# Performance work log

Hardware: AMD Instinct MI355X
Metric: run time of the kernel (lower is better)

## Reference

```python
import jax, jax.numpy as jnp
import numpy as np

N, E, R, H = 20000, 320000, 8, 4
KG, CC = 128, 4
IN, HID, OUT = 256, 256, 256  # in_channels = KG + 128 (GCN out)
HO1, HO2 = HID // H, OUT // H  # per-head out channels
SLOPE_ACT = 0.01   # nn.LeakyReLU default
SLOPE_ATT = 0.2    # RGATConv negative_slope default


def gcn_conv(x, W, b, src, dst):
    """PyG GCNConv: add self loops, symmetric norm, x@W, scatter-sum, +bias."""
    n = x.shape[0]
    loop = jnp.arange(n, dtype=src.dtype)
    s = jnp.concatenate([src, loop])
    d = jnp.concatenate([dst, loop])
    deg = jnp.zeros((n,), x.dtype).at[d].add(1.0)
    dis = jnp.where(deg > 0, jax.lax.rsqrt(jnp.maximum(deg, 1.0)), 0.0)
    norm = dis[s] * dis[d]                        # [E+N]
    h = x @ W                                     # [n, out]
    out = jax.ops.segment_sum(norm[:, None] * h[s], d, num_segments=n)
    return out + b


def rgat_conv(x, W, q, k, b, src, dst, edge_type, heads, oc):
    """PyG RGATConv (additive-self-attention, across-relation, dim=1, concat)."""
    n = x.shape[0]
    xw = jnp.einsum('ni,rio->rno', x, W)          # [R, n, heads*oc]
    out_i = xw[edge_type, dst]                    # [E, heads*oc]
    out_j = xw[edge_type, src]                    # [E, heads*oc]
    qi = out_i @ q                                # [E, heads]
    kj = out_j @ k                                # [E, heads]
    alpha = jax.nn.leaky_relu(qi + kj, SLOPE_ATT)
    # softmax over incoming edges per destination node (across-relation)
    amax = jax.ops.segment_max(alpha, dst, num_segments=n)[dst]
    ex = jnp.exp(alpha - amax)
    denom = jax.ops.segment_sum(ex, dst, num_segments=n)[dst]
    alpha = ex / denom                            # [E, heads]
    e = src.shape[0]
    msg = (alpha[:, :, None] * out_j.reshape(e, heads, oc)).reshape(e, heads * oc)
    out = jax.ops.segment_sum(msg, dst, num_segments=n) + b
    return out, alpha


def setup_inputs() -> dict:
    key = jax.random.key(0)
    ks = jax.random.split(key, 16)
    d = {}
    d['kg_emb'] = jax.random.normal(ks[0], (N, KG), jnp.float32)
    d['ccle0'] = jax.random.normal(ks[1], (N, CC), jnp.float32)
    d['gcn_w1'] = jax.random.normal(ks[2], (CC, 32), jnp.float32) / np.float32(np.sqrt(CC))
    d['gcn_b1'] = jnp.zeros((32,), jnp.float32)
    d['gcn_w2'] = jax.random.normal(ks[3], (32, 128), jnp.float32) / np.float32(np.sqrt(32))
    d['gcn_b2'] = jnp.zeros((128,), jnp.float32)
    d['rgat1_w'] = jax.random.normal(ks[4], (R, IN, HID), jnp.float32) / np.float32(np.sqrt(IN))
    d['rgat1_q'] = jax.random.normal(ks[5], (HID, H), jnp.float32) / np.float32(np.sqrt(HID))
    d['rgat1_k'] = jax.random.normal(ks[6], (HID, H), jnp.float32) / np.float32(np.sqrt(HID))
    d['rgat1_b'] = jnp.zeros((HID,), jnp.float32)
    d['rgat2_w'] = jax.random.normal(ks[7], (R, HID, OUT), jnp.float32) / np.float32(np.sqrt(HID))
    d['rgat2_q'] = jax.random.normal(ks[8], (OUT, H), jnp.float32) / np.float32(np.sqrt(OUT))
    d['rgat2_k'] = jax.random.normal(ks[9], (OUT, H), jnp.float32) / np.float32(np.sqrt(OUT))
    d['rgat2_b'] = jnp.zeros((OUT,), jnp.float32)
    d['lin_w'] = jax.random.normal(ks[10], (IN, OUT), jnp.float32) / np.float32(np.sqrt(IN))
    d['lin_b'] = jnp.zeros((OUT,), jnp.float32)
    d['edge_index'] = jax.random.randint(ks[11], (2, E), 0, N, jnp.int32)
    d['edge_type'] = jax.random.randint(ks[12], (E,), 0, R, jnp.int32)
    return d


def reference(kg_emb, ccle0, gcn_w1, gcn_b1, gcn_w2, gcn_b2,
              rgat1_w, rgat1_q, rgat1_k, rgat1_b,
              rgat2_w, rgat2_q, rgat2_k, rgat2_b,
              lin_w, lin_b, edge_index, edge_type):
    src, dst = edge_index[0], edge_index[1]
    # ccle_layer: GCN(4->32) -> LeakyReLU -> GCN(32->128)
    c = gcn_conv(ccle0, gcn_w1, gcn_b1, src, dst)
    c = jax.nn.leaky_relu(c, SLOPE_ACT)
    c = gcn_conv(c, gcn_w2, gcn_b2, src, dst)
    # node_id = arange(N): concat(kg_emb, ccle_out)
    x0 = jnp.concatenate([kg_emb, c], axis=1)     # [N, IN]
    h, a1 = rgat_conv(x0, rgat1_w, rgat1_q, rgat1_k, rgat1_b,
                      src, dst, edge_type, H, HO1)
    h = jax.nn.leaky_relu(h, SLOPE_ACT)           # dropout p=0 -> identity
    h, a2 = rgat_conv(h, rgat2_w, rgat2_q, rgat2_k, rgat2_b,
                      src, dst, edge_type, H, HO2)
    out = h + (x0 @ lin_w + lin_b)                # residual through self.lin
    return out, a1, a2
```

## Files before the change

### kernel.cpp

```cpp
#include <hip/hip_runtime.h>
#include <cstdint>

static constexpr int N = 20000;
static constexpr int E = 320000;
static constexpr int R = 8;
static constexpr int H = 4;
static constexpr int C = 256;

using short8 = __attribute__((ext_vector_type(8))) short;
using f32x4  = __attribute__((ext_vector_type(4))) float;
using us4    = __attribute__((ext_vector_type(4))) unsigned short;

__device__ __forceinline__ float lrelu(float x, float s) { return x >= 0.f ? x : s * x; }
__device__ __forceinline__ unsigned short f2bf(float f) {
    unsigned u = __float_as_uint(f);
    unsigned r = (u + 0x7FFFu + ((u >> 16) & 1u)) >> 16;
    return (unsigned short)r;
}
__device__ __forceinline__ float bf2f(unsigned short s) {
    return __uint_as_float(((unsigned)s) << 16);
}

__device__ __forceinline__ void gl2l16(const unsigned short* g, unsigned short* l) {
    __builtin_amdgcn_global_load_lds(
        (const __attribute__((address_space(1))) unsigned int*)g,
        (__attribute__((address_space(3))) unsigned int*)l, 16, 0, 0);
}

__global__ void k_zero_int(int* p, int n) {
    int i = blockIdx.x * blockDim.x + threadIdx.x;
    if (i < n) p[i] = 0;
}

__global__ void k_count(const int* __restrict__ ei, int* __restrict__ cnt) {
    int e = blockIdx.x * blockDim.x + threadIdx.x;
    if (e < E) atomicAdd(&cnt[ei[E + e]], 1);
}

__global__ __launch_bounds__(256) void k_scan_a(const int* __restrict__ cnt,
                                                int* __restrict__ loc,
                                                int* __restrict__ bsum) {
    __shared__ int sm[256];
    int t = threadIdx.x;
    int idx = blockIdx.x * 256 + t;
    int v = (idx < N) ? cnt[idx] : 0;
    sm[t] = v;
    __syncthreads();
#pragma unroll
    for (int off = 1; off < 256; off <<= 1) {
        int u = (t >= off) ? sm[t - off] : 0;
        __syncthreads();
        if (t >= off) sm[t] += u;
        __syncthreads();
    }
    if (idx < N) loc[idx] = sm[t] - v;
    if (t == 255) bsum[blockIdx.x] = sm[255];
}

__global__ __launch_bounds__(256) void k_scan_c(const int* __restrict__ cnt,
                                                const int* __restrict__ loc,
                                                const int* __restrict__ bsum,
                                                int* __restrict__ rowptr,
                                                int* __restrict__ cursor,
                                                float* __restrict__ dis) {
    __shared__ int wsum[4];
    __shared__ int smoff;
    int t = threadIdx.x;
    int part = 0;
    for (int j = t; j < blockIdx.x; j += 256) part += bsum[j];
#pragma unroll
    for (int d = 1; d < 64; d <<= 1) part += __shfl_xor(part, d);
    if ((t & 63) == 0) wsum[t >> 6] = part;
    __syncthreads();
    if (t == 0) smoff = wsum[0] + wsum[1] + wsum[2] + wsum[3];
    __syncthreads();
    int base = smoff;
    int idx = blockIdx.x * 256 + t;
    if (idx == 0) rowptr[N] = E;
    if (idx >= N) return;
    int run = base + loc[idx];
    rowptr[idx] = run;
    cursor[idx] = run;
    dis[idx] = rsqrtf((float)cnt[idx] + 1.0f);
}

__global__ void k_scatter(const int* __restrict__ ei, const int* __restrict__ et,
                          int* __restrict__ cursor, int* __restrict__ csr_se,
                          int* __restrict__ csr_eid) {
    int e = blockIdx.x * blockDim.x + threadIdx.x;
    if (e >= E) return;
    int d = ei[E + e];
    int pos = atomicAdd(&cursor[d], 1);
    csr_se[pos] = (et[e] << 16) | ei[e];
    csr_eid[pos] = e;
}

__global__ void k_h1(const float* __restrict__ x, const float* __restrict__ W,
                     float* __restrict__ h) {
    int idx = blockIdx.x * blockDim.x + threadIdx.x;
    if (idx >= N * 32) return;
    int n = idx >> 5, f = idx & 31;
    const float* xr = x + n * 4;
    float acc = 0.f;
#pragma unroll
    for (int c = 0; c < 4; ++c) acc += xr[c] * W[c * 32 + f];
    h[idx] = acc;
}

__global__ void k_agg32(const int* __restrict__ rowptr, const int* __restrict__ csr_se,
                        const float* __restrict__ dis, const float* __restrict__ h,
                        const float* __restrict__ b, float* __restrict__ c) {
    int idx = blockIdx.x * blockDim.x + threadIdx.x;
    if (idx >= N * 32) return;
    int d = idx >> 5, f = idx & 31;
    int beg = rowptr[d], end = rowptr[d + 1];
    float acc = 0.f;
    for (int i = beg; i < end; ++i) {
        int s = csr_se[i] & 0xFFFF;
        acc += dis[s] * h[s * 32 + f];
    }
    float dd = dis[d];
    c[idx] = dd * acc + dd * dd * h[idx] + b[f];
}

__global__ void k_h2kg(const float* __restrict__ c1, const float* __restrict__ W,
                       const float* __restrict__ kg, unsigned short* __restrict__ h,
                       float* __restrict__ x0, unsigned short* __restrict__ xb0) {
    int idx = blockIdx.x * blockDim.x + threadIdx.x;
    if (idx >= N * 128) return;
    int n = idx >> 7, f = idx & 127;
    const float* cr = c1 + n * 32;
    float acc = 0.f;
    for (int c = 0; c < 32; ++c) acc += lrelu(cr[c], 0.01f) * W[c * 128 + f];
    h[idx] = f2bf(acc);
    float v = kg[idx];
    x0[n * 256 + f] = v;
    xb0[n * 256 + f] = f2bf(v);
}

__global__ void k_agg128(const int* __restrict__ rowptr, const int* __restrict__ csr_se,
                         const float* __restrict__ dis,
                         const unsigned short* __restrict__ h,
                         const float* __restrict__ b, float* __restrict__ x0,
                         unsigned short* __restrict__ xb0) {
    int idx = blockIdx.x * blockDim.x + threadIdx.x;
    if (idx >= N * 128) return;
    int d = idx >> 7, f = idx & 127;
    int beg = rowptr[d], end = rowptr[d + 1];
    float acc = 0.f;
    int i = beg;
    for (; i + 2 <= end; i += 2) {
        int s0 = csr_se[i] & 0xFFFF;
        int s1 = csr_se[i + 1] & 0xFFFF;
        float d0 = dis[s0], d1 = dis[s1];
        float v0 = bf2f(h[s0 * 128 + f]), v1 = bf2f(h[s1 * 128 + f]);
        acc += d0 * v0 + d1 * v1;
    }
    if (i < end) {
        int s = csr_se[i] & 0xFFFF;
        acc += dis[s] * bf2f(h[s * 128 + f]);
    }
    float dd = dis[d];
    float v = dd * acc + dd * dd * bf2f(h[d * 128 + f]) + b[f];
    x0[d * 256 + 128 + f] = v;
    xb0[d * 256 + 128 + f] = f2bf(v);
}

__global__ __launch_bounds__(256) void k_wqkb(const float* __restrict__ W,
                                              const float* __restrict__ q,
                                              const float* __restrict__ kmat,
                                              unsigned short* __restrict__ wqkb) {
    int w = (blockIdx.x * blockDim.x + threadIdx.x) >> 6;
    int lane = threadIdx.x & 63;
    int r = w >> 8, i = w & 255;
    const float* wr = W + ((size_t)(r * 256 + i)) * 256;
    float4 a = *(const float4*)(wr + lane * 4);
    float aq0 = 0.f, aq1 = 0.f, aq2 = 0.f, aq3 = 0.f;
    float ak0 = 0.f, ak1 = 0.f, ak2 = 0.f, ak3 = 0.f;
    int o = lane * 4;
    const float av[4] = {a.x, a.y, a.z, a.w};
#pragma unroll
    for (int j = 0; j < 4; ++j) {
        float4 qv = *(const float4*)(q + (o + j) * 4);
        float4 kv = *(const float4*)(kmat + (o + j) * 4);
        aq0 += av[j] * qv.x; aq1 += av[j] * qv.y;
        aq2 += av[j] * qv.z; aq3 += av[j] * qv.w;
        ak0 += av[j] * kv.x; ak1 += av[j] * kv.y;
        ak2 += av[j] * kv.z; ak3 += av[j] * kv.w;
    }
#pragma unroll
    for (int d = 1; d < 64; d <<= 1) {
        aq0 += __shfl_xor(aq0, d); aq1 += __shfl_xor(aq1, d);
        aq2 += __shfl_xor(aq2, d); aq3 += __shfl_xor(aq3, d);
        ak0 += __shfl_xor(ak0, d); ak1 += __shfl_xor(ak1, d);
        ak2 += __shfl_xor(ak2, d); ak3 += __shfl_xor(ak3, d);
    }
    if (lane == 0) {
        int nq = r * 4, nk = 32 + r * 4;
        wqkb[(nq + 0) * 256 + i] = f2bf(aq0);
        wqkb[(nq + 1) * 256 + i] = f2bf(aq1);
        wqkb[(nq + 2) * 256 + i] = f2bf(aq2);
        wqkb[(nq + 3) * 256 + i] = f2bf(aq3);
        wqkb[(nk + 0) * 256 + i] = f2bf(ak0);
        wqkb[(nk + 1) * 256 + i] = f2bf(ak1);
        wqkb[(nk + 2) * 256 + i] = f2bf(ak2);
        wqkb[(nk + 3) * 256 + i] = f2bf(ak3);
    }
}

#define QP 264
__global__ __launch_bounds__(256) void k_qnkn_mfma(
    const unsigned short* __restrict__ xb, const unsigned short* __restrict__ wqkb,
    float* __restrict__ qn, float* __restrict__ kn)
{
    __shared__ unsigned short Ws[64 * QP];
    int t = threadIdx.x;
    {
        int r = t >> 2, off = (t & 3) * 64;
#pragma unroll
        for (int i = 0; i < 8; ++i)
            *(uint4*)(&Ws[r * QP + off + i * 8]) =
                *(const uint4*)(wqkb + r * 256 + off + i * 8);
    }
    __syncthreads();
    int wave = t >> 6, lane = t & 63;
    int lrow = lane & 15, kq = lane >> 4;
    int mw = blockIdx.x * 64 + wave * 16;
    int gm = mw + lrow;
    int gmc = gm < N ? gm : N - 1;

    f32x4 acc[4];
#pragma unroll
    for (int j = 0; j < 4; ++j) acc[j] = (f32x4){0.f, 0.f, 0.f, 0.f};

    for (int k0 = 0; k0 < 8; ++k0) {
        short8 af = *(const short8*)(xb + (size_t)gmc * 256 + k0 * 32 + kq * 8);
#pragma unroll
        for (int j = 0; j < 4; ++j) {
            short8 bf4 = *(const short8*)(&Ws[(j * 16 + lrow) * QP + k0 * 32 + kq * 8]);
            acc[j] = __builtin_amdgcn_mfma_f32_16x16x32_bf16(bf4, af, acc[j], 0, 0, 0);
        }
    }
    if (gm < N) {
#pragma unroll
        for (int j = 0; j < 4; ++j) {
            int colb = j * 16 + kq * 4;
            float4 v = {acc[j][0], acc[j][1], acc[j][2], acc[j][3]};
            if (colb < 32) *(float4*)(qn + (size_t)gm * 32 + colb) = v;
            else           *(float4*)(kn + (size_t)gm * 32 + (colb - 32)) = v;
        }
    }
}

__global__ void k_soft(const int* __restrict__ rowptr, const int* __restrict__ csr_se,
                       const int* __restrict__ csr_eid,
                       const float* __restrict__ qn, const float* __restrict__ kn,
                       float* __restrict__ alpha_csr, float* __restrict__ aout) {
    int wid = (blockIdx.x * blockDim.x + threadIdx.x) >> 6;
    int lane = threadIdx.x & 63;
    if (wid >= N) return;
    int d = wid;
    int beg = rowptr[d], end = rowptr[d + 1];
    if (beg >= end) return;
    int slot = lane >> 2, h = lane & 3;
    int nc = (end - beg + 15) >> 4;
    const float* qrow = qn + d * 32;

    auto rawv = [&](int i) {
        int se = csr_se[i];
        int tt = se >> 16, s = se & 0xFFFF;
        return lrelu(qrow[tt * 4 + h] + kn[s * 32 + tt * 4 + h], 0.2f);
    };

    float av[4];
    float m = -1e30f;
    for (int c = 0; c < nc; ++c) {
        int i = beg + c * 16 + slot;
        float v = (i < end) ? rawv(i) : -1e30f;
        if (c < 4) av[c] = v;
        m = fmaxf(m, v);
    }
    m = fmaxf(m, __shfl_xor(m, 4));
    m = fmaxf(m, __shfl_xor(m, 8));
    m = fmaxf(m, __shfl_xor(m, 16));
    m = fmaxf(m, __shfl_xor(m, 32));

    float sum = 0.f;
    for (int c = 0; c < nc; ++c) {
        int i = beg + c * 16 + slot;
        float ex = 0.f;
        if (i < end) {
            float v = (c < 4) ? av[c] : rawv(i);
            ex = expf(v - m);
        }
        if (c < 4) av[c] = ex;
        sum += ex;
    }
    sum += __shfl_xor(sum, 4);
    sum += __shfl_xor(sum, 8);
    sum += __shfl_xor(sum, 16);
    sum += __shfl_xor(sum, 32);
    float inv = 1.f / sum;

    for (int c = 0; c < nc; ++c) {
        int i = beg + c * 16 + slot;
        if (i < end) {
            float ex = (c < 4) ? av[c] : expf(rawv(i) - m);
            float a = ex * inv;
            alpha_csr[i * 4 + h] = a;
            aout[csr_eid[i] * 4 + h] = a;
        }
    }
}

__global__ __launch_bounds__(256) void k_soft_gather(
    const int* __restrict__ rowptr, const int* __restrict__ csr_se,
    const int* __restrict__ csr_eid,
    const float* __restrict__ qn, const float* __restrict__ kn,
    const unsigned short* __restrict__ xw,
    const float* __restrict__ bias, float* __restrict__ out,
    unsigned short* __restrict__ xbout, float* __restrict__ aout,
    int first, int act)
{
    int node = blockIdx.x * 4 + (threadIdx.x >> 6);
    if (node >= N) return;
    int lane = threadIdx.x & 63;
    int slot = lane >> 2, h = lane & 3;
    int hsel = lane >> 4;
    int beg = rowptr[node], end = rowptr[node + 1];
    float ax = 0.f, ay = 0.f, az = 0.f, aw = 0.f;
    const unsigned short* xwl = xw + lane * 4;

    if (beg < end) {
        int nc = (end - beg + 15) >> 4;
        const float* qrow = qn + node * 32;
        auto rawv = [&](int i) {
            int se = csr_se[i];
            int tt = se >> 16, s = se & 0xFFFF;
            return lrelu(qrow[tt * 4 + h] + kn[s * 32 + tt * 4 + h], 0.2f);
        };

        float av[4];
        float m = -1e30f;
        for (int c = 0; c < nc; ++c) {
            int i = beg + c * 16 + slot;
            float v = (i < end) ? rawv(i) : -1e30f;
            if (c < 4) av[c] = v;
            m = fmaxf(m, v);
        }
        m = fmaxf(m, __shfl_xor(m, 4));
        m = fmaxf(m, __shfl_xor(m, 8));
        m = fmaxf(m, __shfl_xor(m, 16));
        m = fmaxf(m, __shfl_xor(m, 32));

        float sum = 0.f;
        for (int c = 0; c < nc; ++c) {
            int i = beg + c * 16 + slot;
            float ex = 0.f;
            if (i < end) {
                float v = (c < 4) ? av[c] : rawv(i);
                ex = expf(v - m);
            }
            if (c < 4) av[c] = ex;
            sum += ex;
        }
        sum += __shfl_xor(sum, 4);
        sum += __shfl_xor(sum, 8);
        sum += __shfl_xor(sum, 16);
        sum += __shfl_xor(sum, 32);
        float inv = 1.f / sum;

        for (int c = 0; c < nc; ++c) {
            int i = beg + c * 16 + slot;
            float a = 0.f;
            int se = 0;
            if (i < end) {
                float ex = (c < 4) ? av[c] : expf(rawv(i) - m);
                a = ex * inv;
                se = csr_se[i];
                aout[csr_eid[i] * 4 + h] = a;
            }
            int ne = end - (beg + c * 16);
            if (ne > 16) ne = 16;
            for (int e = 0; e < ne; ++e) {
                float ag = __shfl(a, (e << 2) | hsel);
                int seg  = __shfl(se, e << 2);
                int tt = seg >> 16, s = seg & 0xFFFF;
                uint2 pv = *(const uint2*)(xwl + ((size_t)tt * N + s) * 256);
                ax += ag * __uint_as_float(pv.x << 16);
                ay += ag * __uint_as_float(pv.x & 0xFFFF0000u);
                az += ag * __uint_as_float(pv.y << 16);
                aw += ag * __uint_as_float(pv.y & 0xFFFF0000u);
            }
        }
    }

    float* o = out + (size_t)node * 256 + lane * 4;
    float vx, vy, vz, vw;
    if (first) {
        float4 b = *(const float4*)(bias + lane * 4);
        vx = ax + b.x; vy = ay + b.y; vz = az + b.z; vw = aw + b.w;
    } else {
        float4 q = *(const float4*)o;
        vx = q.x + ax; vy = q.y + ay; vz = q.z + az; vw = q.w + aw;
    }
    if (act) {
        vx = lrelu(vx, 0.01f); vy = lrelu(vy, 0.01f);
        vz = lrelu(vz, 0.01f); vw = lrelu(vw, 0.01f);
        us4 xv = {f2bf(vx), f2bf(vy), f2bf(vz), f2bf(vw)};
        *(us4*)(xbout + (size_t)node * 256 + lane * 4) = xv;
    }
    float4 v = {vx, vy, vz, vw};
    *(float4*)o = v;
}

#define WTP 72
__global__ __launch_bounds__(256) void k_wconv_t(const float* __restrict__ W,
                                                 unsigned short* __restrict__ Wt) {
    int bid = blockIdx.x;
    int z = bid >> 4;
    int tile = bid & 15;
    int k0 = (tile >> 2) * 64, n0 = (tile & 3) * 64;
    __shared__ unsigned short T[64 * WTP];
    int t = threadIdx.x;
    const float* Wz = W + ((size_t)z << 16);
    int r = t >> 4;
    int cs = (t & 15) * 4;
#pragma unroll
    for (int rr = 0; rr < 4; ++rr) {
        int k = r + rr * 16;
        float4 v = *(const float4*)(Wz + (size_t)(k0 + k) * 256 + n0 + cs);
        T[(cs + 0) * WTP + k] = f2bf(v.x);
        T[(cs + 1) * WTP + k] = f2bf(v.y);
        T[(cs + 2) * WTP + k] = f2bf(v.z);
        T[(cs + 3) * WTP + k] = f2bf(v.w);
    }
    __syncthreads();
    int n = t >> 2, ck = (t & 3) * 16;
    unsigned short* dst = Wt + ((size_t)z << 16) + (size_t)(n0 + n) * 256 + k0 + ck;
    const unsigned short* srcp = T + n * WTP + ck;
    *(uint4*)(dst) = *(const uint4*)(srcp);
    *(uint4*)(dst + 8) = *(const uint4*)(srcp + 8);
}

#define TM 128
#define TN 128
__global__ __launch_bounds__(256) void gemm_mfma4(
    const unsigned short* __restrict__ A, const unsigned short* __restrict__ Bt,
    unsigned short* __restrict__ Cbf, float* __restrict__ Cf,
    const float* __restrict__ bias, const float* __restrict__ bias2,
    int M, int NZ, int NT, int MT, int zlin)
{
    __shared__ unsigned short As[128 * 32];
    __shared__ unsigned short Bs[128 * 32];

    int bi = blockIdx.x;
    int cx = bi & 7;
    int g = bi >> 3;
    int per = NZ * NT;
    int mh = g / per;
    int j  = g % per;
    int mt = mh * 8 + cx;
    if (mt >= MT) return;
    int z  = j % NZ;
    int nb = j / NZ;
    int m0 = mt * TM;
    int n0 = nb * TN;

    const unsigned short* Bz = Bt + ((size_t)z << 16);
    int t = threadIdx.x;
    int wave = t >> 6, lane = t & 63;
    int wr = wave >> 1, wc = wave & 1;
    int lrow = lane & 15, kq = lane >> 4;

    int sr0 = (wave * 2 + 0) * 16 + (lane >> 2);
    int sr1 = (wave * 2 + 1) * 16 + (lane >> 2);
    int sc = (((lane & 3) ^ ((lane >> 3) & 3))) * 8;
    int gm0 = m0 + sr0; if (gm0 >= M) gm0 = M - 1;
    int gm1 = m0 + sr1; if (gm1 >= M) gm1 = M - 1;
    const unsigned short* gA0 = A + (size_t)gm0 * 256 + sc;
    const unsigned short* gA1 = A + (size_t)gm1 * 256 + sc;
    const unsigned short* gB0 = Bz + (size_t)(n0 + sr0) * 256 + sc;
    const unsigned short* gB1 = Bz + (size_t)(n0 + sr1) * 256 + sc;
    unsigned short* lA0 = &As[(wave * 2 + 0) * 512];
    unsigned short* lA1 = &As[(wave * 2 + 1) * 512];
    unsigned short* lB0 = &Bs[(wave * 2 + 0) * 512];
    unsigned short* lB1 = &Bs[(wave * 2 + 1) * 512];

    int rg = (kq ^ ((lrow >> 1) & 3)) * 8;

    f32x4 acc[4][4];
#pragma unroll
    for (int i = 0; i < 4; ++i)
#pragma unroll
        for (int jj = 0; jj < 4; ++jj) acc[i][jj] = (f32x4){0.f, 0.f, 0.f, 0.f};

    for (int k0 = 0; k0 < 256; k0 += 32) {
        gl2l16(gA0 + k0, lA0);
        gl2l16(gA1 + k0, lA1);
        gl2l16(gB0 + k0, lB0);
        gl2l16(gB1 + k0, lB1);
        __syncthreads();
        short8 af[4], bf4[4];
#pragma unroll
        for (int i = 0; i < 4; ++i)
            af[i] = *(const short8*)(&As[(wr * 64 + i * 16 + lrow) * 32 + rg]);
#pragma unroll
        for (int jj = 0; jj < 4; ++jj)
            bf4[jj] = *(const short8*)(&Bs[(wc * 64 + jj * 16 + lrow) * 32 + rg]);
#pragma unroll
        for (int i = 0; i < 4; ++i)
#pragma unroll
            for (int jj = 0; jj < 4; ++jj)
                acc[i][jj] = __builtin_amdgcn_mfma_f32_16x16x32_bf16(bf4[jj], af[i],
                                                                     acc[i][jj], 0, 0, 0);
        __syncthreads();
    }
    if (z == zlin) {
#pragma unroll
        for (int i = 0; i < 4; ++i) {
            int gm = m0 + wr * 64 + i * 16 + lrow;
            if (gm >= M) continue;
#pragma unroll
            for (int jj = 0; jj < 4; ++jj) {
                int gnb = n0 + wc * 64 + jj * 16 + kq * 4;
                float4 b1 = *(const float4*)(bias + gnb);
                float4 b2 = *(const float4*)(bias2 + gnb);
                float4 v = {acc[i][jj][0] + b1.x + b2.x,
                            acc[i][jj][1] + b1.y + b2.y,
                            acc[i][jj][2] + b1.z + b2.z,
                            acc[i][jj][3] + b1.w + b2.w};
                *(float4*)(Cf + (size_t)gm * 256 + gnb) = v;
            }
        }
    } else {
#pragma unroll
        for (int i = 0; i < 4; ++i) {
            int gm = m0 + wr * 64 + i * 16 + lrow;
            if (gm >= M) continue;
#pragma unroll
            for (int jj = 0; jj < 4; ++jj) {
                int gnb = n0 + wc * 64 + jj * 16 + kq * 4;
                us4 v = {f2bf(acc[i][jj][0]), f2bf(acc[i][jj][1]),
                         f2bf(acc[i][jj][2]), f2bf(acc[i][jj][3])};
                *(us4*)(Cbf + ((size_t)z * M + gm) * 256 + gnb) = v;
            }
        }
    }
}

__global__ __launch_bounds__(256) void k_msg_gather(
    const int* __restrict__ rowptr, const int* __restrict__ csr_se,
    const float* __restrict__ alpha_csr, const unsigned short* __restrict__ xw,
    const float* __restrict__ bias, float* __restrict__ out,
    unsigned short* __restrict__ xbout, int r0, int r1, int first, int act) {
    int node = blockIdx.x * 4 + (threadIdx.x >> 6);
    if (node >= N) return;
    int lane = threadIdx.x & 63;
    int hsel = lane >> 4;
    int beg = rowptr[node], end = rowptr[node + 1];
    float ax = 0.f, ay = 0.f, az = 0.f, aw = 0.f;
    const unsigned short* xwl = xw + lane * 4;

    for (int i = beg; i < end; ++i) {
        int se = csr_se[i];
        int tt = se >> 16;
        if (tt >= r0 && tt < r1) {
            int s = se & 0xFFFF;
            float a = alpha_csr[i * 4 + hsel];
            uint2 pv = *(const uint2*)(xwl + ((size_t)(tt - r0) * N + s) * 256);
            ax += a * __uint_as_float(pv.x << 16);
            ay += a * __uint_as_float(pv.x & 0xFFFF0000u);
            az += a * __uint_as_float(pv.y << 16);
            aw += a * __uint_as_float(pv.y & 0xFFFF0000u);
        }
    }

    float* o = out + (size_t)node * 256 + lane * 4;
    float vx, vy, vz, vw;
    if (first) {
        float4 b = *(const float4*)(bias + lane * 4);
        vx = ax + b.x; vy = ay + b.y; vz = az + b.z; vw = aw + b.w;
    } else {
        float4 q = *(const float4*)o;
        vx = q.x + ax; vy = q.y + ay; vz = q.z + az; vw = q.w + aw;
    }
    if (act) {
        vx = lrelu(vx, 0.01f); vy = lrelu(vy, 0.01f);
        vz = lrelu(vz, 0.01f); vw = lrelu(vw, 0.01f);
        us4 xv = {f2bf(vx), f2bf(vy), f2bf(vz), f2bf(vw)};
        *(us4*)(xbout + (size_t)node * 256 + lane * 4) = xv;
    }
    float4 v = {vx, vy, vz, vw};
    *(float4*)o = v;
}

extern "C" void kernel_launch(void* const* d_in, const int* in_sizes, int n_in,
                              void* d_out, int out_size, void* d_ws, size_t ws_size,
                              hipStream_t stream) {
    const float* kg   = (const float*)d_in[0];
    const float* cc0  = (const float*)d_in[1];
    const float* gw1  = (const float*)d_in[2];
    const float* gb1  = (const float*)d_in[3];
    const float* gw2  = (const float*)d_in[4];
    const float* gb2  = (const float*)d_in[5];
    const float* r1w  = (const float*)d_in[6];
    const float* r1q  = (const float*)d_in[7];
    const float* r1k  = (const float*)d_in[8];
    const float* r1b  = (const float*)d_in[9];
    const float* r2w  = (const float*)d_in[10];
    const float* r2q  = (const float*)d_in[11];
    const float* r2k  = (const float*)d_in[12];
    const float* r2b  = (const float*)d_in[13];
    const float* linw = (const float*)d_in[14];
    const float* linb = (const float*)d_in[15];
    const int*   ei   = (const int*)d_in[16];
    const int*   et   = (const int*)d_in[17];

    float* out = (float*)d_out;
    float* a1  = out + (size_t)N * C;
    float* a2  = a1 + (size_t)E * H;

    float* ws = (float*)d_ws;
    size_t off = 0;
    float* dis  = ws + off; off += N;
    float* h1   = ws + off; off += (size_t)N * 32;
    float* c1   = ws + off; off += (size_t)N * 32;
    unsigned short* h2b = (unsigned short*)(ws + off); off += (size_t)N * 64;
    float* x0   = ws + off; off += (size_t)N * C;
    float* hmid = ws + off; off += (size_t)N * C;
    float* qn   = ws + off; off += (size_t)N * R * H;
    float* kn   = ws + off; off += (size_t)N * R * H;
    int* cnt     = (int*)(ws + off); off += N;
    int* rowptr  = (int*)(ws + off); off += N + 1;
    int* cursor  = (int*)(ws + off); off += N;
    int* scanloc = (int*)(ws + off); off += N;
    int* scanbs  = (int*)(ws + off); off += 256;
    int* csr_se  = (int*)(ws + off); off += E;
    int* csr_eid = (int*)(ws + off); off += E;
    float* alpha = ws + off; off += (size_t)E * H;
    unsigned short* xb0 = (unsigned short*)(ws + off); off += (size_t)N * 128;
    unsigned short* xb1 = (unsigned short*)(ws + off); off += (size_t)N * 128;
    unsigned short* wt  = (unsigned short*)(ws + off); off += (size_t)(R + 1) * 32768;
    unsigned short* wtl = wt + ((size_t)R << 16);
    unsigned short* wqkb = (unsigned short*)(ws + off); off += 8192;
    unsigned short* xwb = (unsigned short*)(ws + off);

    size_t fixedB = off * 4;
    int K = R;
    if (ws_size > fixedB) {
        size_t kmax = (ws_size - fixedB) / ((size_t)N * C * 2);
        if (kmax < (size_t)K) K = (int)kmax;
    } else {
        K = 1;
    }
    if (K < 1) K = 1;

    const int B = 256;
    auto cdiv = [](long a, long b) { return (int)((a + b - 1) / b); };
    const int MT = cdiv(N, TM);
    const int NT = C / TN;
    const int NB = cdiv(N, 256);

    k_zero_int<<<cdiv(N, B), B, 0, stream>>>(cnt, N);
    k_count<<<cdiv(E, B), B, 0, stream>>>(ei, cnt);
    k_scan_a<<<NB, 256, 0, stream>>>(cnt, scanloc, scanbs);
    k_scan_c<<<NB, 256, 0, stream>>>(cnt, scanloc, scanbs, rowptr, cursor, dis);
    k_scatter<<<cdiv(E, B), B, 0, stream>>>(ei, et, cursor, csr_se, csr_eid);

    k_h1<<<cdiv((long)N * 32, B), B, 0, stream>>>(cc0, gw1, h1);
    k_agg32<<<cdiv((long)N * 32, B), B, 0, stream>>>(rowptr, csr_se, dis, h1, gb1, c1);
    k_h2kg<<<cdiv((long)N * 128, B), B, 0, stream>>>(c1, gw2, kg, h2b, x0, xb0);
    k_agg128<<<cdiv((long)N * 128, B), B, 0, stream>>>(rowptr, csr_se, dis, h2b,
                                                       gb2, x0, xb0);

    auto rgat = [&](unsigned short* xb, const float* W,
                    const float* q, const float* kk, const float* b,
                    float* obuf, unsigned short* xbout, float* aout,
                    int first, int act, int lin, float* linout,
                    const float* lb1, const float* lb2) {
        k_wqkb<<<512, 256, 0, stream>>>(W, q, kk, wqkb);
        k_qnkn_mfma<<<cdiv(N, 64), B, 0, stream>>>(xb, wqkb, qn, kn);
        k_wconv_t<<<R * 16, 256, 0, stream>>>(W, wt);
        if (K == R) {
            int nz = R + (lin ? 1 : 0);
            int zl = lin ? R : -1;
            int gx = 8 * nz * NT * cdiv(MT, 8);
            gemm_mfma4<<<gx, 512 / 2, 0, stream>>>(xb, wt, xwb, linout, lb1, lb2,
                                                   N, nz, NT, MT, zl);
            k_soft_gather<<<cdiv(N, 4), B, 0, stream>>>(
                rowptr, csr_se, csr_eid, qn, kn, xwb, b, obuf, xbout, aout,
                first, act);
        } else {
            k_soft<<<cdiv((long)N * 64, B), B, 0, stream>>>(rowptr, csr_se, csr_eid,
                                                            qn, kn, alpha, aout);
            for (int r0 = 0; r0 < R; r0 += K) {
                int kc = (R - r0) < K ? (R - r0) : K;
                int addlin = (lin && (r0 + kc == R)) ? 1 : 0;
                int nz = kc + addlin;
                int zl = addlin ? kc : -1;
                int gx = 8 * nz * NT * cdiv(MT, 8);
                gemm_mfma4<<<gx, 256, 0, stream>>>(xb, wt + ((size_t)r0 << 16), xwb,
                                                   linout, lb1, lb2,
                                                   N, nz, NT, MT, zl);
                int last = (r0 + kc >= R) ? 1 : 0;
                k_msg_gather<<<cdiv(N, 4), 256, 0, stream>>>(
                    rowptr, csr_se, alpha, xwb, b, obuf, xbout, r0, r0 + kc,
                    (first && r0 == 0) ? 1 : 0, act && last);
            }
        }
    };

    k_wconv_t<<<16, 256, 0, stream>>>(linw, wtl);

    rgat(xb0, r1w, r1q, r1k, r1b, hmid, xb1, a1, 1, 1,
         1, out, linb, r2b);

    rgat(xb1, r2w, r2q, r2k, r2b, out, nullptr, a2, 0, 0,
         0, nullptr, nullptr, nullptr);
}
```

Before: 455.2 us.

## Merge prep kernels into one launch and unroll soft-gather edge loop by four

Folds the zeroing of counts, the first GCN feature transform, all weight bf16 transposes for both RGAT layers and the linear layer, and both q/k weight projections into a single block-dispatched prep kernel. This removes several small kernel launches and the serialization between them. The soft-gather kernel now caches the packed source/type word from the first pass instead of reloading it. Its aggregation loop processes four edges per iteration so the independent gathers can be in flight together, at the cost of extra registers and a separate second-layer weight buffer.

New measurement: 436.1 us (median of 2 runs). 1.04x faster.

```diff
diff --git a/kernel.cpp b/kernel.cpp
--- a/kernel.cpp
+++ b/kernel.cpp
@@ -27,9 +27,116 @@
         (__attribute__((address_space(3))) unsigned int*)l, 16, 0, 0);
 }
 
-__global__ void k_zero_int(int* p, int n) {
-    int i = blockIdx.x * blockDim.x + threadIdx.x;
-    if (i < n) p[i] = 0;
+#define WTP 72
+
+__device__ __forceinline__ void wconv_body(const float* __restrict__ W,
+                                           unsigned short* __restrict__ Wt,
+                                           int bid, unsigned short* T) {
+    int z = bid >> 4;
+    int tile = bid & 15;
+    int k0 = (tile >> 2) * 64, n0 = (tile & 3) * 64;
+    int t = threadIdx.x;
+    const float* Wz = W + ((size_t)z << 16);
+    int r = t >> 4;
+    int cs = (t & 15) * 4;
+#pragma unroll
+    for (int rr = 0; rr < 4; ++rr) {
+        int k = r + rr * 16;
+        float4 v = *(const float4*)(Wz + (size_t)(k0 + k) * 256 + n0 + cs);
+        T[(cs + 0) * WTP + k] = f2bf(v.x);
+        T[(cs + 1) * WTP + k] = f2bf(v.y);
+        T[(cs + 2) * WTP + k] = f2bf(v.z);
+        T[(cs + 3) * WTP + k] = f2bf(v.w);
+    }
+    __syncthreads();
+    int n = t >> 2, ck = (t & 3) * 16;
+    unsigned short* dst = Wt + ((size_t)z << 16) + (size_t)(n0 + n) * 256 + k0 + ck;
+    const unsigned short* srcp = T + n * WTP + ck;
+    *(uint4*)(dst) = *(const uint4*)(srcp);
+    *(uint4*)(dst + 8) = *(const uint4*)(srcp + 8);
+}
+
+__device__ __forceinline__ void wqkb_body(const float* __restrict__ W,
+                                          const float* __restrict__ q,
+                                          const float* __restrict__ kmat,
+                                          unsigned short* __restrict__ wqkb,
+                                          int w) {
+    int lane = threadIdx.x & 63;
+    int r = w >> 8, i = w & 255;
+    const float* wr = W + ((size_t)(r * 256 + i)) * 256;
+    float4 a = *(const float4*)(wr + lane * 4);
+    float aq0 = 0.f, aq1 = 0.f, aq2 = 0.f, aq3 = 0.f;
+    float ak0 = 0.f, ak1 = 0.f, ak2 = 0.f, ak3 = 0.f;
+    int o = lane * 4;
+    const float av[4] = {a.x, a.y, a.z, a.w};
+#pragma unroll
+    for (int j = 0; j < 4; ++j) {
+        float4 qv = *(const float4*)(q + (o + j) * 4);
+        float4 kv = *(const float4*)(kmat + (o + j) * 4);
+        aq0 += av[j] * qv.x; aq1 += av[j] * qv.y;
+        aq2 += av[j] * qv.z; aq3 += av[j] * qv.w;
+        ak0 += av[j] * kv.x; ak1 += av[j] * kv.y;
+        ak2 += av[j] * kv.z; ak3 += av[j] * kv.w;
+    }
+#pragma unroll
+    for (int d = 1; d < 64; d <<= 1) {
+        aq0 += __shfl_xor(aq0, d); aq1 += __shfl_xor(aq1, d);
+        aq2 += __shfl_xor(aq2, d); aq3 += __shfl_xor(aq3, d);
+        ak0 += __shfl_xor(ak0, d); ak1 += __shfl_xor(ak1, d);
+        ak2 += __shfl_xor(ak2, d); ak3 += __shfl_xor(ak3, d);
+    }
+    if (lane == 0) {
+        int nq = r * 4, nk = 32 + r * 4;
+        wqkb[(nq + 0) * 256 + i] = f2bf(aq0);
+        wqkb[(nq + 1) * 256 + i] = f2bf(aq1);
+        wqkb[(nq + 2) * 256 + i] = f2bf(aq2);
+        wqkb[(nq + 3) * 256 + i] = f2bf(aq3);
+        wqkb[(nk + 0) * 256 + i] = f2bf(ak0);
+        wqkb[(nk + 1) * 256 + i] = f2bf(ak1);
+        wqkb[(nk + 2) * 256 + i] = f2bf(ak2);
+        wqkb[(nk + 3) * 256 + i] = f2bf(ak3);
+    }
+}
+
+__global__ __launch_bounds__(256) void k_prep(
+    int* __restrict__ cnt,
+    const float* __restrict__ cc0, const float* __restrict__ gw1,
+    float* __restrict__ h1buf,
+    const float* __restrict__ r1w, const float* __restrict__ r2w,
+    const float* __restrict__ linw,
+    unsigned short* __restrict__ wt, unsigned short* __restrict__ wt2,
+    const float* __restrict__ r1q, const float* __restrict__ r1k,
+    unsigned short* __restrict__ wqkb1,
+    const float* __restrict__ r2q, const float* __restrict__ r2k,
+    unsigned short* __restrict__ wqkb2)
+{
+    __shared__ unsigned short T[64 * WTP];
+    int b = blockIdx.x;
+    int t = threadIdx.x;
+    if (b < 79) {
+        int idx = b * 256 + t;
+        if (idx < N) cnt[idx] = 0;
+    } else if (b < 2579) {
+        int idx = (b - 79) * 256 + t;
+        if (idx < N * 32) {
+            int n = idx >> 5, f = idx & 31;
+            const float* xr = cc0 + n * 4;
+            float acc = 0.f;
+#pragma unroll
+            for (int c = 0; c < 4; ++c) acc += xr[c] * gw1[c * 32 + f];
+            h1buf[idx] = acc;
+        }
+    } else if (b < 2707) {
+        wconv_body(r1w, wt, b - 2579, T);
+    } else if (b < 2835) {
+        wconv_body(r2w, wt2, b - 2707, T);
+    } else if (b < 2851) {
+        wconv_body(linw, wt + ((size_t)R << 16), b - 2835, T);
+    } else if (b < 3363) {
+        wqkb_body(r1w, r1q, r1k, wqkb1, ((b - 2851) * 256 + t) >> 6);
+    } else {
+        wqkb_body(r2w, r2q, r2k, wqkb2, ((b - 3363) * 256 + t) >> 6);
+    }
 }
 
 __global__ void k_count(const int* __restrict__ ei, int* __restrict__ cnt) {
@@ -93,18 +200,6 @@
     int pos = atomicAdd(&cursor[d], 1);
     csr_se[pos] = (et[e] << 16) | ei[e];
     csr_eid[pos] = e;
-}
-
-__global__ void k_h1(const float* __restrict__ x, const float* __restrict__ W,
-                     float* __restrict__ h) {
-    int idx = blockIdx.x * blockDim.x + threadIdx.x;
-    if (idx >= N * 32) return;
-    int n = idx >> 5, f = idx & 31;
-    const float* xr = x + n * 4;
-    float acc = 0.f;
-#pragma unroll
-    for (int c = 0; c < 4; ++c) acc += xr[c] * W[c * 32 + f];
-    h[idx] = acc;
 }
 
 __global__ void k_agg32(const int* __restrict__ rowptr, const int* __restrict__ csr_se,
@@ -166,48 +261,6 @@
     xb0[d * 256 + 128 + f] = f2bf(v);
 }
 
-__global__ __launch_bounds__(256) void k_wqkb(const float* __restrict__ W,
-                                              const float* __restrict__ q,
-                                              const float* __restrict__ kmat,
-                                              unsigned short* __restrict__ wqkb) {
-    int w = (blockIdx.x * blockDim.x + threadIdx.x) >> 6;
-    int lane = threadIdx.x & 63;
-    int r = w >> 8, i = w & 255;
-    const float* wr = W + ((size_t)(r * 256 + i)) * 256;
-    float4 a = *(const float4*)(wr + lane * 4);
-    float aq0 = 0.f, aq1 = 0.f, aq2 = 0.f, aq3 = 0.f;
-    float ak0 = 0.f, ak1 = 0.f, ak2 = 0.f, ak3 = 0.f;
-    int o = lane * 4;
-    const float av[4] = {a.x, a.y, a.z, a.w};
-#pragma unroll
-    for (int j = 0; j < 4; ++j) {
-        float4 qv = *(const float4*)(q + (o + j) * 4);
-        float4 kv = *(const float4*)(kmat + (o + j) * 4);
-        aq0 += av[j] * qv.x; aq1 += av[j] * qv.y;
-        aq2 += av[j] * qv.z; aq3 += av[j] * qv.w;
-        ak0 += av[j] * kv.x; ak1 += av[j] * kv.y;
-        ak2 += av[j] * kv.z; ak3 += av[j] * kv.w;
-    }
-#pragma unroll
-    for (int d = 1; d < 64; d <<= 1) {
-        aq0 += __shfl_xor(aq0, d); aq1 += __shfl_xor(aq1, d);
-        aq2 += __shfl_xor(aq2, d); aq3 += __shfl_xor(aq3, d);
-        ak0 += __shfl_xor(ak0, d); ak1 += __shfl_xor(ak1, d);
-        ak2 += __shfl_xor(ak2, d); ak3 += __shfl_xor(ak3, d);
-    }
-    if (lane == 0) {
-        int nq = r * 4, nk = 32 + r * 4;
-        wqkb[(nq + 0) * 256 + i] = f2bf(aq0);
-        wqkb[(nq + 1) * 256 + i] = f2bf(aq1);
-        wqkb[(nq + 2) * 256 + i] = f2bf(aq2);
-        wqkb[(nq + 3) * 256 + i] = f2bf(aq3);
-        wqkb[(nk + 0) * 256 + i] = f2bf(ak0);
-        wqkb[(nk + 1) * 256 + i] = f2bf(ak1);
-        wqkb[(nk + 2) * 256 + i] = f2bf(ak2);
-        wqkb[(nk + 3) * 256 + i] = f2bf(ak3);
-    }
-}
-
 #define QP 264
 __global__ __launch_bounds__(256) void k_qnkn_mfma(
     const unsigned short* __restrict__ xb, const unsigned short* __restrict__ wqkb,
@@ -334,18 +387,18 @@
     if (beg < end) {
         int nc = (end - beg + 15) >> 4;
         const float* qrow = qn + node * 32;
-        auto rawv = [&](int i) {
-            int se = csr_se[i];
+        auto rawv_se = [&](int se) {
             int tt = se >> 16, s = se & 0xFFFF;
             return lrelu(qrow[tt * 4 + h] + kn[s * 32 + tt * 4 + h], 0.2f);
         };
 
-        float av[4];
+        float av[4]; int sev[4];
         float m = -1e30f;
         for (int c = 0; c < nc; ++c) {
             int i = beg + c * 16 + slot;
-            float v = (i < end) ? rawv(i) : -1e30f;
-            if (c < 4) av[c] = v;
+            float v = -1e30f; int se = 0;
+            if (i < end) { se = csr_se[i]; v = rawv_se(se); }
+            if (c < 4) { av[c] = v; sev[c] = se; }
             m = fmaxf(m, v);
         }
         m = fmaxf(m, __shfl_xor(m, 4));
@@ -358,7 +411,7 @@
             int i = beg + c * 16 + slot;
             float ex = 0.f;
             if (i < end) {
-                float v = (c < 4) ? av[c] : rawv(i);
+                float v = (c < 4) ? av[c] : rawv_se(csr_se[i]);
                 ex = expf(v - m);
             }
             if (c < 4) av[c] = ex;
@@ -375,22 +428,47 @@
             float a = 0.f;
             int se = 0;
             if (i < end) {
-                float ex = (c < 4) ? av[c] : expf(rawv(i) - m);
+                float ex;
+                if (c < 4) { ex = av[c]; se = sev[c]; }
+                else       { se = csr_se[i]; ex = expf(rawv_se(se) - m); }
                 a = ex * inv;
-                se = csr_se[i];
                 aout[csr_eid[i] * 4 + h] = a;
             }
             int ne = end - (beg + c * 16);
             if (ne > 16) ne = 16;
-            for (int e = 0; e < ne; ++e) {
-                float ag = __shfl(a, (e << 2) | hsel);
-                int seg  = __shfl(se, e << 2);
-                int tt = seg >> 16, s = seg & 0xFFFF;
-                uint2 pv = *(const uint2*)(xwl + ((size_t)tt * N + s) * 256);
-                ax += ag * __uint_as_float(pv.x << 16);
-                ay += ag * __uint_as_float(pv.x & 0xFFFF0000u);
-                az += ag * __uint_as_float(pv.y << 16);
-                aw += ag * __uint_as_float(pv.y & 0xFFFF0000u);
+            for (int e = 0; e < ne; e += 4) {
+                int rr = ne - e;
+                int e1 = (rr > 1) ? e + 1 : e;
+                int e2 = (rr > 2) ? e + 2 : e;
+                int e3 = (rr > 3) ? e + 3 : e;
+                float ag0 = __shfl(a, (e  << 2) | hsel);
+                float ag1 = __shfl(a, (e1 << 2) | hsel); if (rr <= 1) ag1 = 0.f;
+                float ag2 = __shfl(a, (e2 << 2) | hsel); if (rr <= 2) ag2 = 0.f;
+                float ag3 = __shfl(a, (e3 << 2) | hsel); if (rr <= 3) ag3 = 0.f;
+                int sg0 = __shfl(se, e  << 2);
+                int sg1 = __shfl(se, e1 << 2);
+                int sg2 = __shfl(se, e2 << 2);
+                int sg3 = __shfl(se, e3 << 2);
+                uint2 v0 = *(const uint2*)(xwl + ((size_t)(sg0 >> 16) * N + (sg0 & 0xFFFF)) * 256);
+                uint2 v1 = *(const uint2*)(xwl + ((size_t)(sg1 >> 16) * N + (sg1 & 0xFFFF)) * 256);
+                uint2 v2 = *(const uint2*)(xwl + ((size_t)(sg2 >> 16) * N + (sg2 & 0xFFFF)) * 256);
+                uint2 v3 = *(const uint2*)(xwl + ((size_t)(sg3 >> 16) * N + (sg3 & 0xFFFF)) * 256);
+                ax += ag0 * __uint_as_float(v0.x << 16);
+                ay += ag0 * __uint_as_float(v0.x & 0xFFFF0000u);
+                az += ag0 * __uint_as_float(v0.y << 16);
+                aw += ag0 * __uint_as_float(v0.y & 0xFFFF0000u);
+                ax += ag1 * __uint_as_float(v1.x << 16);
+                ay += ag1 * __uint_as_float(v1.x & 0xFFFF0000u);
+                az += ag1 * __uint_as_float(v1.y << 16);
+                aw += ag1 * __uint_as_float(v1.y & 0xFFFF0000u);
+                ax += ag2 * __uint_as_float(v2.x << 16);
+                ay += ag2 * __uint_as_float(v2.x & 0xFFFF0000u);
+                az += ag2 * __uint_as_float(v2.y << 16);
+                aw += ag2 * __uint_as_float(v2.y & 0xFFFF0000u);
+                ax += ag3 * __uint_as_float(v3.x << 16);
+                ay += ag3 * __uint_as_float(v3.x & 0xFFFF0000u);
+                az += ag3 * __uint_as_float(v3.y << 16);
+                aw += ag3 * __uint_as_float(v3.y & 0xFFFF0000u);
             }
         }
     }
@@ -412,35 +490,6 @@
     }
     float4 v = {vx, vy, vz, vw};
     *(float4*)o = v;
-}
-
-#define WTP 72
-__global__ __launch_bounds__(256) void k_wconv_t(const float* __restrict__ W,
-                                                 unsigned short* __restrict__ Wt) {
-    int bid = blockIdx.x;
-    int z = bid >> 4;
-    int tile = bid & 15;
-    int k0 = (tile >> 2) * 64, n0 = (tile & 3) * 64;
-    __shared__ unsigned short T[64 * WTP];
-    int t = threadIdx.x;
-    const float* Wz = W + ((size_t)z << 16);
-    int r = t >> 4;
-    int cs = (t & 15) * 4;
-#pragma unroll
-    for (int rr = 0; rr < 4; ++rr) {
-        int k = r + rr * 16;
-        float4 v = *(const float4*)(Wz + (size_t)(k0 + k) * 256 + n0 + cs);
-        T[(cs + 0) * WTP + k] = f2bf(v.x);
-        T[(cs + 1) * WTP + k] = f2bf(v.y);
-        T[(cs + 2) * WTP + k] = f2bf(v.z);
-        T[(cs + 3) * WTP + k] = f2bf(v.w);
-    }
-    __syncthreads();
-    int n = t >> 2, ck = (t & 3) * 16;
-    unsigned short* dst = Wt + ((size_t)z << 16) + (size_t)(n0 + n) * 256 + k0 + ck;
-    const unsigned short* srcp = T + n * WTP + ck;
-    *(uint4*)(dst) = *(const uint4*)(srcp);
-    *(uint4*)(dst + 8) = *(const uint4*)(srcp + 8);
 }
 
 #define TM 128
@@ -642,8 +691,10 @@
     unsigned short* xb0 = (unsigned short*)(ws + off); off += (size_t)N * 128;
     unsigned short* xb1 = (unsigned short*)(ws + off); off += (size_t)N * 128;
     unsigned short* wt  = (unsigned short*)(ws + off); off += (size_t)(R + 1) * 32768;
+    unsigned short* wt2 = (unsigned short*)(ws + off); off += (size_t)R * 32768;
     unsigned short* wtl = wt + ((size_t)R << 16);
-    unsigned short* wqkb = (unsigned short*)(ws + off); off += 8192;
+    unsigned short* wqkb1 = (unsigned short*)(ws + off); off += 8192;
+    unsigned short* wqkb2 = (unsigned short*)(ws + off); off += 8192;
     unsigned short* xwb = (unsigned short*)(ws + off);
 
     size_t fixedB = off * 4;
@@ -662,32 +713,32 @@
     const int NT = C / TN;
     const int NB = cdiv(N, 256);
 
-    k_zero_int<<<cdiv(N, B), B, 0, stream>>>(cnt, N);
+    k_prep<<<3875, 256, 0, stream>>>(cnt, cc0, gw1, h1,
+                                     r1w, r2w, linw, wt, wt2,
+                                     r1q, r1k, wqkb1, r2q, r2k, wqkb2);
+
     k_count<<<cdiv(E, B), B, 0, stream>>>(ei, cnt);
     k_scan_a<<<NB, 256, 0, stream>>>(cnt, scanloc, scanbs);
     k_scan_c<<<NB, 256, 0, stream>>>(cnt, scanloc, scanbs, rowptr, cursor, dis);
     k_scatter<<<cdiv(E, B), B, 0, stream>>>(ei, et, cursor, csr_se, csr_eid);
 
-    k_h1<<<cdiv((long)N * 32, B), B, 0, stream>>>(cc0, gw1, h1);
     k_agg32<<<cdiv((long)N * 32, B), B, 0, stream>>>(rowptr, csr_se, dis, h1, gb1, c1);
     k_h2kg<<<cdiv((long)N * 128, B), B, 0, stream>>>(c1, gw2, kg, h2b, x0, xb0);
     k_agg128<<<cdiv((long)N * 128, B), B, 0, stream>>>(rowptr, csr_se, dis, h2b,
                                                        gb2, x0, xb0);
 
-    auto rgat = [&](unsigned short* xb, const float* W,
-                    const float* q, const float* kk, const float* b,
+    auto rgat = [&](unsigned short* xb, const unsigned short* wqkb_l,
+                    const unsigned short* wt_l, const float* b,
                     float* obuf, unsigned short* xbout, float* aout,
                     int first, int act, int lin, float* linout,
                     const float* lb1, const float* lb2) {
-        k_wqkb<<<512, 256, 0, stream>>>(W, q, kk, wqkb);
-        k_qnkn_mfma<<<cdiv(N, 64), B, 0, stream>>>(xb, wqkb, qn, kn);
-        k_wconv_t<<<R * 16, 256, 0, stream>>>(W, wt);
+        k_qnkn_mfma<<<cdiv(N, 64), B, 0, stream>>>(xb, wqkb_l, qn, kn);
         if (K == R) {
             int nz = R + (lin ? 1 : 0);
             int zl = lin ? R : -1;
             int gx = 8 * nz * NT * cdiv(MT, 8);
-            gemm_mfma4<<<gx, 512 / 2, 0, stream>>>(xb, wt, xwb, linout, lb1, lb2,
-                                                   N, nz, NT, MT, zl);
+            gemm_mfma4<<<gx, 256, 0, stream>>>(xb, wt_l, xwb, linout, lb1, lb2,
+                                               N, nz, NT, MT, zl);
             k_soft_gather<<<cdiv(N, 4), B, 0, stream>>>(
                 rowptr, csr_se, csr_eid, qn, kn, xwb, b, obuf, xbout, aout,
                 first, act);
@@ -700,7 +751,7 @@
                 int nz = kc + addlin;
                 int zl = addlin ? kc : -1;
                 int gx = 8 * nz * NT * cdiv(MT, 8);
-                gemm_mfma4<<<gx, 256, 0, stream>>>(xb, wt + ((size_t)r0 << 16), xwb,
+                gemm_mfma4<<<gx, 256, 0, stream>>>(xb, wt_l + ((size_t)r0 << 16), xwb,
                                                    linout, lb1, lb2,
                                                    N, nz, NT, MT, zl);
                 int last = (r0 + kc >= R) ? 1 : 0;
@@ -711,11 +762,9 @@
         }
     };
 
-    k_wconv_t<<<16, 256, 0, stream>>>(linw, wtl);
-
-    rgat(xb0, r1w, r1q, r1k, r1b, hmid, xb1, a1, 1, 1,
+    rgat(xb0, wqkb1, wt, r1b, hmid, xb1, a1, 1, 1,
          1, out, linb, r2b);
 
-    rgat(xb1, r2w, r2q, r2k, r2b, out, nullptr, a2, 0, 0,
+    rgat(xb1, wqkb2, wt2, r2b, out, nullptr, a2, 0, 0,
          0, nullptr, nullptr, nullptr);
 }
```
